# Kernel optimization log

Hardware: AMD Instinct MI355X
Metric: run time of the kernel (lower is better)

Reference implementation:

```python
import jax, jax.numpy as jnp
import numpy as np

B = 4096
FEATURE_SIZE = 64 * 64 * 10  # 40960 (HalfKP)
H1, H2, H3 = 256, 32, 32
NNZ = 30  # ~pieces on board per side


def _onehot_multi(key, batch, dim, nnz):
    # Build sparse feature vectors: nnz ones scattered per row (matches HalfKP usage).
    idx = jax.random.randint(key, (batch, nnz), 0, dim)
    x = jnp.zeros((batch, dim), dtype=jnp.float32)
    rows = jnp.arange(batch)[:, None]
    return x.at[rows, idx].set(1.0)


def setup_inputs() -> dict:
    key = jax.random.key(0)
    kw, kb, k1, k2, k3, k4, k5 = jax.random.split(key, 7)
    # xavier_uniform with gain=0.5: bound = 0.5 * sqrt(6/(fan_in+fan_out))
    def xavier(k, out_f, in_f):
        bound = 0.5 * np.sqrt(6.0 / (in_f + out_f))
        return jax.random.uniform(k, (out_f, in_f), jnp.float32, -bound, bound)
    return {
        "white_features": _onehot_multi(kw, B, FEATURE_SIZE, NNZ),
        "black_features": _onehot_multi(kb, B, FEATURE_SIZE, NNZ),
        "ft_w": xavier(k1, H1, FEATURE_SIZE),
        "ft_b": jnp.zeros((H1,), jnp.float32),
        "fc1_w": xavier(k2, H2, 2 * H1),
        "fc1_b": jnp.zeros((H2,), jnp.float32),
        "fc2_w": xavier(k3, H3, H2),
        "fc2_b": jnp.zeros((H3,), jnp.float32),
        "fc3_w": xavier(k4, 1, H3),
        "fc3_b": jnp.zeros((1,), jnp.float32),
    }


def _crelu(x):
    return jnp.clip(x, 0.0, 1.0)


def reference(white_features, black_features, ft_w, ft_b, fc1_w, fc1_b,
              fc2_w, fc2_b, fc3_w, fc3_b):
    # feature transform (dense equivalent of sparse gather-sum)
    w = _crelu(white_features @ ft_w.T + ft_b)  # [B, 256]
    b = _crelu(black_features @ ft_w.T + ft_b)  # [B, 256]
    x = jnp.concatenate([w, b], axis=1)          # [B, 512]
    x = _crelu(x @ fc1_w.T + fc1_b)              # [B, 32]
    x = _crelu(x @ fc2_w.T + fc2_b)              # [B, 32]
    return x @ fc3_w.T + fc3_b                   # [B, 1]
```

## Files before the change

kernel.cpp:

```cpp
#include <hip/hip_runtime.h>
#include <hip/hip_bf16.h>

#define FEAT 40960
#define NH1  256
#define MAXNZ 128

typedef float vfloat4 __attribute__((ext_vector_type(4)));

__global__ __launch_bounds__(256) void transpose_ftw(const float* __restrict__ ft_w,
                                                     float* __restrict__ ft_wt) {
    __shared__ float tile[32][33];
    const int i0 = blockIdx.x * 32;
    const int h0 = blockIdx.y * 32;
    const int tx = threadIdx.x;
    const int ty = threadIdx.y;
#pragma unroll
    for (int j = 0; j < 4; ++j) {
        tile[ty + j * 8][tx] = ft_w[(size_t)(h0 + ty + j * 8) * FEAT + i0 + tx];
    }
    __syncthreads();
#pragma unroll
    for (int j = 0; j < 4; ++j) {
        ft_wt[(size_t)(i0 + ty + j * 8) * NH1 + h0 + tx] = tile[tx][ty + j * 8];
    }
}

__global__ __launch_bounds__(256) void nnue_fused(
    const float* __restrict__ wf,
    const float* __restrict__ bfeat,
    const float* __restrict__ ft_wt,
    const float* __restrict__ ft_b,
    const float* __restrict__ fc1_w,
    const float* __restrict__ fc1_b,
    const float* __restrict__ fc2_w,
    const float* __restrict__ fc2_b,
    const float* __restrict__ fc3_w,
    const float* __restrict__ fc3_b,
    float* __restrict__ out)
{
    __shared__ int   idxw[MAXNZ], idxb[MAXNZ];
    __shared__ float valw[MAXNZ], valb[MAXNZ];
    __shared__ int   cntw, cntb;
    __shared__ float xsh[512];
    __shared__ float red[256];
    __shared__ float h1[32], h2[32];

    const int tid = threadIdx.x;
    const int b   = blockIdx.x;

    if (tid == 0) { cntw = 0; cntb = 0; }
    __syncthreads();

    const vfloat4* wf4 = (const vfloat4*)(wf    + (size_t)b * FEAT);
    const vfloat4* bf4 = (const vfloat4*)(bfeat + (size_t)b * FEAT);
    constexpr int ITERS = FEAT / 4 / 256;
#pragma unroll 4
    for (int it = 0; it < ITERS; ++it) {
        const int k4 = it * 256 + tid;
        const vfloat4 vw = __builtin_nontemporal_load(wf4 + k4);
        const vfloat4 vb = __builtin_nontemporal_load(bf4 + k4);
        const int base = k4 * 4;
        const bool anyw = (vw.x != 0.f) | (vw.y != 0.f) | (vw.z != 0.f) | (vw.w != 0.f);
        const bool anyb = (vb.x != 0.f) | (vb.y != 0.f) | (vb.z != 0.f) | (vb.w != 0.f);
        if (__any(anyw)) {
            if (vw.x != 0.f) { int p = atomicAdd(&cntw, 1); if (p < MAXNZ) { idxw[p] = base + 0; valw[p] = vw.x; } }
            if (vw.y != 0.f) { int p = atomicAdd(&cntw, 1); if (p < MAXNZ) { idxw[p] = base + 1; valw[p] = vw.y; } }
            if (vw.z != 0.f) { int p = atomicAdd(&cntw, 1); if (p < MAXNZ) { idxw[p] = base + 2; valw[p] = vw.z; } }
            if (vw.w != 0.f) { int p = atomicAdd(&cntw, 1); if (p < MAXNZ) { idxw[p] = base + 3; valw[p] = vw.w; } }
        }
        if (__any(anyb)) {
            if (vb.x != 0.f) { int p = atomicAdd(&cntb, 1); if (p < MAXNZ) { idxb[p] = base + 0; valb[p] = vb.x; } }
            if (vb.y != 0.f) { int p = atomicAdd(&cntb, 1); if (p < MAXNZ) { idxb[p] = base + 1; valb[p] = vb.y; } }
            if (vb.z != 0.f) { int p = atomicAdd(&cntb, 1); if (p < MAXNZ) { idxb[p] = base + 2; valb[p] = vb.z; } }
            if (vb.w != 0.f) { int p = atomicAdd(&cntb, 1); if (p < MAXNZ) { idxb[p] = base + 3; valb[p] = vb.w; } }
        }
    }
    __syncthreads();
    const int nw = min(cntw, MAXNZ);
    const int nb = min(cntb, MAXNZ);

    float aw0 = ft_b[tid], aw1 = 0.f;
    float ab0 = aw0,       ab1 = 0.f;
    const int nmin = min(nw, nb);
    int j = 0;
    for (; j + 2 <= nmin; j += 2) {
        const float w0 = ft_wt[(size_t)idxw[j]     * NH1 + tid];
        const float w1 = ft_wt[(size_t)idxw[j + 1] * NH1 + tid];
        const float b0 = ft_wt[(size_t)idxb[j]     * NH1 + tid];
        const float b1 = ft_wt[(size_t)idxb[j + 1] * NH1 + tid];
        aw0 += valw[j] * w0;  aw1 += valw[j + 1] * w1;
        ab0 += valb[j] * b0;  ab1 += valb[j + 1] * b1;
    }
    for (int jw = j; jw < nw; ++jw) aw0 += valw[jw] * ft_wt[(size_t)idxw[jw] * NH1 + tid];
    for (int jb = j; jb < nb; ++jb) ab0 += valb[jb] * ft_wt[(size_t)idxb[jb] * NH1 + tid];

    xsh[tid]       = fminf(fmaxf(aw0 + aw1, 0.f), 1.f);
    xsh[256 + tid] = fminf(fmaxf(ab0 + ab1, 0.f), 1.f);
    __syncthreads();

    {
        const int o = tid & 31, part = tid >> 5;
        const float* wrow = fc1_w + o * 512 + part * 64;
        const float* xp   = xsh + part * 64;
        float s = 0.f;
#pragma unroll
        for (int k = 0; k < 64; ++k) s += wrow[k] * xp[k];
        red[tid] = s;
    }
    __syncthreads();
    if (tid < 32) {
        float s = fc1_b[tid];
#pragma unroll
        for (int p = 0; p < 8; ++p) s += red[tid + p * 32];
        h1[tid] = fminf(fmaxf(s, 0.f), 1.f);
    }
    __syncthreads();

    if (tid < 32) {
        float s = fc2_b[tid];
#pragma unroll
        for (int k = 0; k < 32; ++k) s += fc2_w[tid * 32 + k] * h1[k];
        h2[tid] = fminf(fmaxf(s, 0.f), 1.f);
    }
    __syncthreads();

    if (tid == 0) {
        float s = fc3_b[0];
#pragma unroll
        for (int k = 0; k < 32; ++k) s += fc3_w[k] * h2[k];
        out[b] = s;
    }
}

extern "C" void kernel_launch(void* const* d_in, const int* in_sizes, int n_in,
                              void* d_out, int out_size, void* d_ws, size_t ws_size,
                              hipStream_t stream) {
    const float* wf    = (const float*)d_in[0];
    const float* bfeat = (const float*)d_in[1];
    const float* ft_w  = (const float*)d_in[2];
    const float* ft_b  = (const float*)d_in[3];
    const float* fc1_w = (const float*)d_in[4];
    const float* fc1_b = (const float*)d_in[5];
    const float* fc2_w = (const float*)d_in[6];
    const float* fc2_b = (const float*)d_in[7];
    const float* fc3_w = (const float*)d_in[8];
    const float* fc3_b = (const float*)d_in[9];
    float* out = (float*)d_out;

    const int B = in_sizes[0] / FEAT;
    float* ft_wt = (float*)d_ws;

    {
        dim3 blk(32, 8);
        dim3 grd(FEAT / 32, NH1 / 32);
        transpose_ftw<<<grd, blk, 0, stream>>>(ft_w, ft_wt);
    }
    nnue_fused<<<B, 256, 0, stream>>>(wf, bfeat, ft_wt,
                                      ft_b, fc1_w, fc1_b, fc2_w, fc2_b,
                                      fc3_w, fc3_b, out);
}
```

Measured before the change: 1.243 ms.

## Split sparse-feature scan into grid-wide kernel feeding separate MLP kernel

Moves the dense scan for nonzero features out of the per-row fused kernel into a separate grid-stride kernel over the whole input, with global atomics building per-row index/value lists in workspace. The MLP kernel then just loads these lists. The aim is better streaming bandwidth on the 1.3 GB dense input, since it is no longer tied to one block per row. In exchange it adds two kernel launches and global atomic traffic, and the per-row capacity drops from 128 to 64 nonzeros.

```diff
diff --git a/kernel.cpp b/kernel.cpp
--- a/kernel.cpp
+++ b/kernel.cpp
@@ -3,9 +3,14 @@
 
 #define FEAT 40960
 #define NH1  256
-#define MAXNZ 128
+#define CAP  64
 
 typedef float vfloat4 __attribute__((ext_vector_type(4)));
+
+__global__ __launch_bounds__(256) void zero_cnt(int* __restrict__ cnt, int n) {
+    const int i = blockIdx.x * 256 + threadIdx.x;
+    if (i < n) cnt[i] = 0;
+}
 
 __global__ __launch_bounds__(256) void transpose_ftw(const float* __restrict__ ft_w,
                                                      float* __restrict__ ft_wt) {
@@ -15,19 +20,49 @@
     const int tx = threadIdx.x;
     const int ty = threadIdx.y;
 #pragma unroll
-    for (int j = 0; j < 4; ++j) {
+    for (int j = 0; j < 4; ++j)
         tile[ty + j * 8][tx] = ft_w[(size_t)(h0 + ty + j * 8) * FEAT + i0 + tx];
-    }
     __syncthreads();
 #pragma unroll
-    for (int j = 0; j < 4; ++j) {
+    for (int j = 0; j < 4; ++j)
         ft_wt[(size_t)(i0 + ty + j * 8) * NH1 + h0 + tx] = tile[tx][ty + j * 8];
+}
+
+__global__ __launch_bounds__(256) void scan_nz(
+    const float* __restrict__ wf,
+    const float* __restrict__ bfeat,
+    int*   __restrict__ cnt,
+    int*   __restrict__ idxl,
+    float* __restrict__ vall,
+    int B)
+{
+    const int side = blockIdx.y;
+    const vfloat4* base4 = (const vfloat4*)(side == 0 ? wf : bfeat);
+    int* scnt = cnt + side * B;
+    int* sidx = idxl + (size_t)side * B * CAP;
+    float* sval = vall + (size_t)side * B * CAP;
+
+    const size_t nf4 = (size_t)B * FEAT / 4;
+    const size_t gstride = (size_t)gridDim.x * 256;
+    for (size_t i4 = blockIdx.x * 256 + threadIdx.x; i4 < nf4; i4 += gstride) {
+        const vfloat4 v = __builtin_nontemporal_load(base4 + i4);
+        const bool any = (v.x != 0.f) | (v.y != 0.f) | (v.z != 0.f) | (v.w != 0.f);
+        if (__any(any)) {
+            const int e = (int)(i4 * 4);
+            const int r = e / FEAT;
+            const int c = e - r * FEAT;
+            if (v.x != 0.f) { int p = atomicAdd(&scnt[r], 1); if (p < CAP) { sidx[r * CAP + p] = c + 0; sval[r * CAP + p] = v.x; } }
+            if (v.y != 0.f) { int p = atomicAdd(&scnt[r], 1); if (p < CAP) { sidx[r * CAP + p] = c + 1; sval[r * CAP + p] = v.y; } }
+            if (v.z != 0.f) { int p = atomicAdd(&scnt[r], 1); if (p < CAP) { sidx[r * CAP + p] = c + 2; sval[r * CAP + p] = v.z; } }
+            if (v.w != 0.f) { int p = atomicAdd(&scnt[r], 1); if (p < CAP) { sidx[r * CAP + p] = c + 3; sval[r * CAP + p] = v.w; } }
+        }
     }
 }
 
-__global__ __launch_bounds__(256) void nnue_fused(
-    const float* __restrict__ wf,
-    const float* __restrict__ bfeat,
+__global__ __launch_bounds__(256) void nnue_mlp(
+    const int*   __restrict__ cnt,
+    const int*   __restrict__ idxl,
+    const float* __restrict__ vall,
     const float* __restrict__ ft_wt,
     const float* __restrict__ ft_b,
     const float* __restrict__ fc1_w,
@@ -36,11 +71,11 @@
     const float* __restrict__ fc2_b,
     const float* __restrict__ fc3_w,
     const float* __restrict__ fc3_b,
-    float* __restrict__ out)
+    float* __restrict__ out,
+    int B)
 {
-    __shared__ int   idxw[MAXNZ], idxb[MAXNZ];
-    __shared__ float valw[MAXNZ], valb[MAXNZ];
-    __shared__ int   cntw, cntb;
+    __shared__ int   idxw[CAP], idxb[CAP];
+    __shared__ float valw[CAP], valb[CAP];
     __shared__ float xsh[512];
     __shared__ float red[256];
     __shared__ float h1[32], h2[32];
@@ -48,36 +83,15 @@
     const int tid = threadIdx.x;
     const int b   = blockIdx.x;
 
-    if (tid == 0) { cntw = 0; cntb = 0; }
-    __syncthreads();
-
-    const vfloat4* wf4 = (const vfloat4*)(wf    + (size_t)b * FEAT);
-    const vfloat4* bf4 = (const vfloat4*)(bfeat + (size_t)b * FEAT);
-    constexpr int ITERS = FEAT / 4 / 256;
-#pragma unroll 4
-    for (int it = 0; it < ITERS; ++it) {
-        const int k4 = it * 256 + tid;
-        const vfloat4 vw = __builtin_nontemporal_load(wf4 + k4);
-        const vfloat4 vb = __builtin_nontemporal_load(bf4 + k4);
-        const int base = k4 * 4;
-        const bool anyw = (vw.x != 0.f) | (vw.y != 0.f) | (vw.z != 0.f) | (vw.w != 0.f);
-        const bool anyb = (vb.x != 0.f) | (vb.y != 0.f) | (vb.z != 0.f) | (vb.w != 0.f);
-        if (__any(anyw)) {
-            if (vw.x != 0.f) { int p = atomicAdd(&cntw, 1); if (p < MAXNZ) { idxw[p] = base + 0; valw[p] = vw.x; } }
-            if (vw.y != 0.f) { int p = atomicAdd(&cntw, 1); if (p < MAXNZ) { idxw[p] = base + 1; valw[p] = vw.y; } }
-            if (vw.z != 0.f) { int p = atomicAdd(&cntw, 1); if (p < MAXNZ) { idxw[p] = base + 2; valw[p] = vw.z; } }
-            if (vw.w != 0.f) { int p = atomicAdd(&cntw, 1); if (p < MAXNZ) { idxw[p] = base + 3; valw[p] = vw.w; } }
-        }
-        if (__any(anyb)) {
-            if (vb.x != 0.f) { int p = atomicAdd(&cntb, 1); if (p < MAXNZ) { idxb[p] = base + 0; valb[p] = vb.x; } }
-            if (vb.y != 0.f) { int p = atomicAdd(&cntb, 1); if (p < MAXNZ) { idxb[p] = base + 1; valb[p] = vb.y; } }
-            if (vb.z != 0.f) { int p = atomicAdd(&cntb, 1); if (p < MAXNZ) { idxb[p] = base + 2; valb[p] = vb.z; } }
-            if (vb.w != 0.f) { int p = atomicAdd(&cntb, 1); if (p < MAXNZ) { idxb[p] = base + 3; valb[p] = vb.w; } }
-        }
+    const int nw = min(cnt[b],     CAP);
+    const int nb = min(cnt[B + b], CAP);
+    if (tid < CAP) {
+        idxw[tid] = idxl[(size_t)b * CAP + tid];
+        valw[tid] = vall[(size_t)b * CAP + tid];
+        idxb[tid] = idxl[(size_t)(B + b) * CAP + tid];
+        valb[tid] = vall[(size_t)(B + b) * CAP + tid];
     }
     __syncthreads();
-    const int nw = min(cntw, MAXNZ);
-    const int nb = min(cntb, MAXNZ);
 
     float aw0 = ft_b[tid], aw1 = 0.f;
     float ab0 = aw0,       ab1 = 0.f;
@@ -148,14 +162,24 @@
     float* out = (float*)d_out;
 
     const int B = in_sizes[0] / FEAT;
-    float* ft_wt = (float*)d_ws;
 
+    char* ws = (char*)d_ws;
+    float* ft_wt = (float*)ws;                       ws += (size_t)FEAT * NH1 * sizeof(float);
+    int*   cnt   = (int*)ws;                         ws += (size_t)2 * B * sizeof(int);
+    int*   idxl  = (int*)ws;                         ws += (size_t)2 * B * CAP * sizeof(int);
+    float* vall  = (float*)ws;
+
+    zero_cnt<<<(2 * B + 255) / 256, 256, 0, stream>>>(cnt, 2 * B);
     {
         dim3 blk(32, 8);
         dim3 grd(FEAT / 32, NH1 / 32);
         transpose_ftw<<<grd, blk, 0, stream>>>(ft_w, ft_wt);
     }
-    nnue_fused<<<B, 256, 0, stream>>>(wf, bfeat, ft_wt,
-                                      ft_b, fc1_w, fc1_b, fc2_w, fc2_b,
-                                      fc3_w, fc3_b, out);
+    {
+        dim3 grd(2048, 2);
+        scan_nz<<<grd, 256, 0, stream>>>(wf, bfeat, cnt, idxl, vall, B);
+    }
+    nnue_mlp<<<B, 256, 0, stream>>>(cnt, idxl, vall, ft_wt,
+                                    ft_b, fc1_w, fc1_b, fc2_w, fc2_b,
+                                    fc3_w, fc3_b, out, B);
 }
```

After: 1.314 ms. 1.06x slower.
